# Kernel optimization log

Hardware: AMD Instinct MI355X
Metric: run time of the kernel (lower is better)

## Reference

```python
import jax, jax.numpy as jnp
import numpy as np

D, NH, NKV, HD, DFF, W, PLD = 2048, 8, 2, 256, 8192, 512, 256
EPS = 1e-6

def rmsnorm(x, w):
    # Gemma-style RMSNorm with (1 + weight) scaling
    return x * jax.lax.rsqrt(jnp.mean(x * x, axis=-1, keepdims=True) + EPS) * (1.0 + w)

def rmsnorm_nw(x):
    # v_norm: weightless RMSNorm
    return x * jax.lax.rsqrt(jnp.mean(x * x, axis=-1, keepdims=True) + EPS)

def rotate_half(x):
    x1, x2 = jnp.split(x, 2, axis=-1)
    return jnp.concatenate([-x2, x1], axis=-1)

def setup_inputs() -> dict:
    key = jax.random.key(0)
    ks = jax.random.split(key, 24)
    w = lambda k, shp, s=0.02: (jax.random.normal(k, shp, dtype=jnp.float32) * s)
    inp = {
        "hidden_states": jax.random.normal(ks[0], (1, 1, D), dtype=jnp.float32),
        "cos": jax.random.uniform(ks[1], (1, 1, HD), dtype=jnp.float32),
        "sin": jax.random.uniform(ks[2], (1, 1, HD), dtype=jnp.float32),
        "mask": jnp.zeros((1, 1, 1, W), dtype=jnp.float32),
        "kv_cache": jnp.zeros((2, NKV, W, HD), dtype=jnp.float32),
        "per_layer": jax.random.normal(ks[3], (1, 1, PLD), dtype=jnp.float32),
        "ln_in_w": w(ks[4], (D,)),
        "Wq": w(ks[5], (NH * HD, D)),
        "q_norm_w": w(ks[6], (HD,)),
        "Wk": w(ks[7], (NKV * HD, D)),
        "Wv": w(ks[8], (NKV * HD, D)),
        "k_norm_w": w(ks[9], (HD,)),
        "Wo": w(ks[10], (D, NH * HD)),
        "post_attn_ln_w": w(ks[11], (D,)),
        "pre_ffn_ln_w": w(ks[12], (D,)),
        "Wgate": w(ks[13], (DFF, D)),
        "Wup": w(ks[14], (DFF, D)),
        "Wdown": w(ks[15], (D, DFF)),
        "post_ffn_ln_w": w(ks[16], (D,)),
        "Wpl_gate": w(ks[17], (PLD, D)),
        "Wpl_proj": w(ks[18], (D, PLD)),
        "post_pl_ln_w": w(ks[19], (D,)),
        "layer_scalar": jnp.ones((1,), dtype=jnp.float32),
        "ring_pos": 37,
    }
    return inp

def reference(hidden_states, cos, sin, mask, kv_cache, per_layer,
              ln_in_w, Wq, q_norm_w, Wk, Wv, k_norm_w, Wo,
              post_attn_ln_w, pre_ffn_ln_w, Wgate, Wup, Wdown, post_ffn_ln_w,
              Wpl_gate, Wpl_proj, post_pl_ln_w, layer_scalar, ring_pos):
    n_rep = NH // NKV
    x = hidden_states[0, 0]                      # (D,)
    residual = x
    h = rmsnorm(x, ln_in_w)                      # input_layernorm
    c, s = cos[0, 0], sin[0, 0]                  # (HD,)
    # q/k/v projections (seq=1 decode -> GEMV)
    q = (h @ Wq.T).reshape(NH, HD)
    q = rmsnorm(q, q_norm_w)
    q = q * c + rotate_half(q) * s               # RoPE
    k = (h @ Wk.T).reshape(NKV, HD)
    k = rmsnorm(k, k_norm_w)
    k = k * c + rotate_half(k) * s
    v = rmsnorm_nw((h @ Wv.T).reshape(NKV, HD))
    # slice-write into the ring-buffer KV cache
    kv = kv_cache.at[0, :, ring_pos, :].set(k).at[1, :, ring_pos, :].set(v)
    K, V = kv[0], kv[1]                          # (NKV, W, HD)
    # GQA: repeat kv heads n_rep times
    Kx = jnp.repeat(K, n_rep, axis=0)            # (NH, W, HD)
    Vx = jnp.repeat(V, n_rep, axis=0)
    scores = jnp.einsum('hd,hwd->hw', q, Kx) + mask[0, 0, 0]   # no 1/sqrt(hd), as in source
    attn = jax.nn.softmax(scores, axis=-1)
    o = jnp.einsum('hw,hwd->hd', attn, Vx).reshape(NH * HD)
    attn_out = rmsnorm(o @ Wo.T, post_attn_ln_w)
    x = residual + attn_out
    # gated-GELU MLP
    residual = x
    hn = rmsnorm(x, pre_ffn_ln_w)
    gate = jax.nn.gelu(hn @ Wgate.T, approximate=True)
    mlp = ((gate * (hn @ Wup.T)) @ Wdown.T)
    x = residual + rmsnorm(mlp, post_ffn_ln_w)
    # per-layer input gate/projection
    residual = x
    g = jax.nn.gelu(x @ Wpl_gate.T, approximate=True) * per_layer[0, 0]
    g = rmsnorm(g @ Wpl_proj.T, post_pl_ln_w)
    x = (residual + g) * layer_scalar[0]
    return x.reshape(1, 1, D)

if __name__ == '__main__':
    out = reference(**setup_inputs())
    print(out.shape, out.dtype)
```

## Files before the change

kernel.cpp:

```cpp
#include <hip/hip_runtime.h>
#include <math.h>

#define D 2048
#define NH 8
#define NKV 2
#define HD 256
#define DFF 8192
#define W 512
#define PLD 256
#define EPS 1e-6f

typedef float f32x4 __attribute__((ext_vector_type(4)));

__device__ __forceinline__ f32x4 ntld(const float* p) {
    return __builtin_nontemporal_load(reinterpret_cast<const f32x4*>(p));
}
__device__ __forceinline__ f32x4 ld4(const float* p) {
    return *reinterpret_cast<const f32x4*>(p);
}
__device__ __forceinline__ float dot4(f32x4 a, f32x4 b, float acc) {
    return fmaf(a.x, b.x, fmaf(a.y, b.y, fmaf(a.z, b.z, fmaf(a.w, b.w, acc))));
}

__device__ __forceinline__ float wave_sum(float v) {
    #pragma unroll
    for (int off = 32; off > 0; off >>= 1) v += __shfl_xor(v, off, 64);
    return v;
}
__device__ __forceinline__ float wave_max(float v) {
    #pragma unroll
    for (int off = 32; off > 0; off >>= 1) v = fmaxf(v, __shfl_xor(v, off, 64));
    return v;
}

__device__ __forceinline__ float gelu_tanh(float x) {
    const float c = 0.7978845608028654f;
    float t = tanhf(c * (x + 0.044715f * x * x * x));
    return 0.5f * x * (1.0f + t);
}

__global__ __launch_bounds__(256, 1)
void qkv_fused(const float* __restrict__ Wq, const float* __restrict__ Wk,
               const float* __restrict__ Wv, const float* __restrict__ x,
               const float* __restrict__ lnw, float* __restrict__ qraw,
               float* __restrict__ kraw, float* __restrict__ vraw) {
    int lane = threadIdx.x & 63, wid = threadIdx.x >> 6;
    int row = blockIdx.x * 4 + wid;
    const float* wr;
    float* outp;
    if (row < 2048)      { wr = Wq + (size_t)row * D;          outp = qraw + row; }
    else if (row < 2560) { wr = Wk + (size_t)(row - 2048) * D; outp = kraw + (row - 2048); }
    else                 { wr = Wv + (size_t)(row - 2560) * D; outp = vraw + (row - 2560); }
    f32x4 xv[8], lw[8];
    #pragma unroll
    for (int c = 0; c < 8; c++) xv[c] = ld4(x + c * 256 + lane * 4);
    #pragma unroll
    for (int c = 0; c < 8; c++) lw[c] = ld4(lnw + c * 256 + lane * 4);
    f32x4 wv4[8];
    #pragma unroll
    for (int c = 0; c < 8; c++) wv4[c] = ntld(wr + c * 256 + lane * 4);
    float ss = 0.f;
    #pragma unroll
    for (int c = 0; c < 8; c++) ss = dot4(xv[c], xv[c], ss);
    ss = wave_sum(ss);
    float rs = rsqrtf(ss / (float)D + EPS);
    float acc = 0.f;
    #pragma unroll
    for (int c = 0; c < 8; c++) {
        f32x4 h4 = xv[c] * rs * (1.f + lw[c]);
        acc = dot4(wv4[c], h4, acc);
    }
    acc = wave_sum(acc);
    if (lane == 0) *outp = acc;
}

__global__ __launch_bounds__(1024, 1)
void attn_fused(const float* __restrict__ kvc, const float* __restrict__ qraw,
                const float* __restrict__ kraw, const float* __restrict__ vraw,
                const float* __restrict__ qw, const float* __restrict__ kw,
                const float* __restrict__ cosv, const float* __restrict__ sinv,
                const float* __restrict__ mask, const int* __restrict__ ring_p,
                float* __restrict__ attn_o) {
    __shared__ float qn[HD], kn[HD], vn[HD], p[W], red[16], oacc[4][HD];
    int t = threadIdx.x, wv = t >> 6, lane = t & 63;
    int head = blockIdx.x, kvh = head >> 2;
    int ring = *ring_p;
    if (wv == 0) {
        f32x4 v4 = ld4(qraw + head * HD + lane * 4);
        float ss = wave_sum(dot4(v4, v4, 0.f));
        float rs = rsqrtf(ss / (float)HD + EPS);
        f32x4 w4 = ld4(qw + lane * 4);
        f32x4 nv = v4 * rs * (1.f + w4);
        f32x4 pr;
        pr.x = __shfl_xor(nv.x, 32, 64);
        pr.y = __shfl_xor(nv.y, 32, 64);
        pr.z = __shfl_xor(nv.z, 32, 64);
        pr.w = __shfl_xor(nv.w, 32, 64);
        f32x4 c4 = ld4(cosv + lane * 4), s4 = ld4(sinv + lane * 4);
        float sgn = (lane < 32) ? -1.f : 1.f;
        f32x4 o4 = nv * c4 + pr * s4 * sgn;
        *reinterpret_cast<f32x4*>(qn + lane * 4) = o4;
    } else if (wv == 1) {
        f32x4 v4 = ld4(kraw + kvh * HD + lane * 4);
        float ss = wave_sum(dot4(v4, v4, 0.f));
        float rs = rsqrtf(ss / (float)HD + EPS);
        f32x4 w4 = ld4(kw + lane * 4);
        f32x4 nv = v4 * rs * (1.f + w4);
        f32x4 pr;
        pr.x = __shfl_xor(nv.x, 32, 64);
        pr.y = __shfl_xor(nv.y, 32, 64);
        pr.z = __shfl_xor(nv.z, 32, 64);
        pr.w = __shfl_xor(nv.w, 32, 64);
        f32x4 c4 = ld4(cosv + lane * 4), s4 = ld4(sinv + lane * 4);
        float sgn = (lane < 32) ? -1.f : 1.f;
        f32x4 o4 = nv * c4 + pr * s4 * sgn;
        *reinterpret_cast<f32x4*>(kn + lane * 4) = o4;
    } else if (wv == 2) {
        f32x4 v4 = ld4(vraw + kvh * HD + lane * 4);
        float ss = wave_sum(dot4(v4, v4, 0.f));
        float rs = rsqrtf(ss / (float)HD + EPS);
        *reinterpret_cast<f32x4*>(vn + lane * 4) = v4 * rs;
    }
    __syncthreads();
    {
        f32x4 qq = *reinterpret_cast<f32x4*>(qn + lane * 4);
        f32x4 krg = *reinterpret_cast<f32x4*>(kn + lane * 4);
        const float* Kb = kvc + (size_t)kvh * W * HD;
        #pragma unroll 4
        for (int i = 0; i < 32; i++) {
            int w = wv * 32 + i;
            f32x4 k4 = (w == ring) ? krg : ld4(Kb + (size_t)w * HD + lane * 4);
            float s = wave_sum(dot4(qq, k4, 0.f));
            if (lane == 0) p[w] = s + mask[w];
        }
    }
    __syncthreads();
    float e = 0.f, sv = 0.f;
    if (t < W) {
        sv = p[t];
        float m = wave_max(sv);
        if (lane == 0) red[wv] = m;
    }
    __syncthreads();
    float m = red[0];
    #pragma unroll
    for (int i = 1; i < 8; i++) m = fmaxf(m, red[i]);
    if (t < W) e = expf(sv - m);
    __syncthreads();
    if (t < W) {
        float se = wave_sum(e);
        if (lane == 0) red[wv] = se;
    }
    __syncthreads();
    float tot = 0.f;
    #pragma unroll
    for (int i = 0; i < 8; i++) tot += red[i];
    if (t < W) p[t] = e / tot;
    __syncthreads();
    {
        int d = t & 255, q = t >> 8;
        float vr = vn[d];
        const float* Vb = kvc + (size_t)(NKV + kvh) * W * HD;
        float acc = 0.f;
        #pragma unroll 8
        for (int i = 0; i < 128; i++) {
            int w = q * 128 + i;
            float vv = (w == ring) ? vr : Vb[(size_t)w * HD + d];
            acc = fmaf(p[w], vv, acc);
        }
        oacc[q][d] = acc;
    }
    __syncthreads();
    if (t < HD) attn_o[head * HD + t] = oacc[0][t] + oacc[1][t] + oacc[2][t] + oacc[3][t];
}

__global__ __launch_bounds__(256, 1)
void gemv2048_nt(const float* __restrict__ Wm, const float* __restrict__ x,
                 float* __restrict__ y) {
    int lane = threadIdx.x & 63, wid = threadIdx.x >> 6;
    int row = blockIdx.x * 4 + wid;
    const float* wr = Wm + (size_t)row * D;
    f32x4 xv[8], w[8];
    #pragma unroll
    for (int c = 0; c < 8; c++) xv[c] = ld4(x + c * 256 + lane * 4);
    #pragma unroll
    for (int c = 0; c < 8; c++) w[c] = ntld(wr + c * 256 + lane * 4);
    float acc = 0.f;
    #pragma unroll
    for (int c = 0; c < 8; c++) acc = dot4(w[c], xv[c], acc);
    acc = wave_sum(acc);
    if (lane == 0) y[row] = acc;
}

__global__ __launch_bounds__(256, 1)
void gateup_fused(const float* __restrict__ Wg, const float* __restrict__ Wu,
                  const float* __restrict__ x, const float* __restrict__ ywo,
                  const float* __restrict__ w_pa, const float* __restrict__ w_pf,
                  float* __restrict__ act, float* __restrict__ x1out) {
    int lane = threadIdx.x & 63, wid = threadIdx.x >> 6;
    int row = blockIdx.x * 4 + wid;
    const float* wg = Wg + (size_t)row * D;
    const float* wu = Wu + (size_t)row * D;
    f32x4 y4[8], xr4[8], w1[8], w2[8];
    #pragma unroll
    for (int c = 0; c < 8; c++) y4[c] = ld4(ywo + c * 256 + lane * 4);
    #pragma unroll
    for (int c = 0; c < 8; c++) xr4[c] = ld4(x + c * 256 + lane * 4);
    #pragma unroll
    for (int c = 0; c < 8; c++) w1[c] = ld4(w_pa + c * 256 + lane * 4);
    #pragma unroll
    for (int c = 0; c < 8; c++) w2[c] = ld4(w_pf + c * 256 + lane * 4);
    f32x4 g4[8], u4[8];
    #pragma unroll
    for (int c = 0; c < 8; c++) g4[c] = ntld(wg + c * 256 + lane * 4);
    #pragma unroll
    for (int c = 0; c < 8; c++) u4[c] = ntld(wu + c * 256 + lane * 4);
    float ss = 0.f;
    #pragma unroll
    for (int c = 0; c < 8; c++) ss = dot4(y4[c], y4[c], ss);
    ss = wave_sum(ss);
    float rs1 = rsqrtf(ss / (float)D + EPS);
    f32x4 x1v[8];
    float s2 = 0.f;
    #pragma unroll
    for (int c = 0; c < 8; c++) {
        f32x4 v = xr4[c] + y4[c] * rs1 * (1.f + w1[c]);
        x1v[c] = v;
        s2 = dot4(v, v, s2);
    }
    s2 = wave_sum(s2);
    float rs2 = rsqrtf(s2 / (float)D + EPS);
    if (blockIdx.x == 0 && wid == 0) {
        #pragma unroll
        for (int c = 0; c < 8; c++)
            *reinterpret_cast<f32x4*>(x1out + c * 256 + lane * 4) = x1v[c];
    }
    float ag = 0.f, au = 0.f;
    #pragma unroll
    for (int c = 0; c < 8; c++) {
        f32x4 h4 = x1v[c] * rs2 * (1.f + w2[c]);
        ag = dot4(g4[c], h4, ag);
        au = dot4(u4[c], h4, au);
    }
    ag = wave_sum(ag);
    au = wave_sum(au);
    if (lane == 0) act[row] = gelu_tanh(ag) * au;
}

__global__ __launch_bounds__(256, 1)
void down_nt(const float* __restrict__ Wd, const float* __restrict__ act,
             float* __restrict__ y) {
    int lane = threadIdx.x & 63, wid = threadIdx.x >> 6;
    int row = blockIdx.x * 4 + wid;
    const float* wr = Wd + (size_t)row * DFF;
    f32x4 wA[8], wB[8], a[8];
    float acc = 0.f;
    #pragma unroll
    for (int c = 0; c < 8; c++) a[c] = ld4(act + c * 256 + lane * 4);
    #pragma unroll
    for (int c = 0; c < 8; c++) wA[c] = ntld(wr + c * 256 + lane * 4);
    #pragma unroll
    for (int c = 0; c < 8; c++) wB[c] = ntld(wr + 2048 + c * 256 + lane * 4);
    #pragma unroll
    for (int c = 0; c < 8; c++) acc = dot4(wA[c], a[c], acc);
    #pragma unroll
    for (int c = 0; c < 8; c++) a[c] = ld4(act + 2048 + c * 256 + lane * 4);
    #pragma unroll
    for (int c = 0; c < 8; c++) wA[c] = ntld(wr + 4096 + c * 256 + lane * 4);
    #pragma unroll
    for (int c = 0; c < 8; c++) acc = dot4(wB[c], a[c], acc);
    #pragma unroll
    for (int c = 0; c < 8; c++) a[c] = ld4(act + 4096 + c * 256 + lane * 4);
    #pragma unroll
    for (int c = 0; c < 8; c++) wB[c] = ntld(wr + 6144 + c * 256 + lane * 4);
    #pragma unroll
    for (int c = 0; c < 8; c++) acc = dot4(wA[c], a[c], acc);
    #pragma unroll
    for (int c = 0; c < 8; c++) a[c] = ld4(act + 6144 + c * 256 + lane * 4);
    #pragma unroll
    for (int c = 0; c < 8; c++) acc = dot4(wB[c], a[c], acc);
    acc = wave_sum(acc);
    if (lane == 0) y[row] = acc;
}

__global__ __launch_bounds__(256, 1)
void plgate_fused(const float* __restrict__ Wpl, const float* __restrict__ x1,
                  const float* __restrict__ y2, const float* __restrict__ w_pf,
                  const float* __restrict__ per_layer, float* __restrict__ g,
                  float* __restrict__ x2out) {
    int lane = threadIdx.x & 63, wid = threadIdx.x >> 6;
    int row = blockIdx.x * 4 + wid;
    f32x4 y4[8], x4[8], w4[8];
    #pragma unroll
    for (int c = 0; c < 8; c++) y4[c] = ld4(y2 + c * 256 + lane * 4);
    #pragma unroll
    for (int c = 0; c < 8; c++) x4[c] = ld4(x1 + c * 256 + lane * 4);
    #pragma unroll
    for (int c = 0; c < 8; c++) w4[c] = ld4(w_pf + c * 256 + lane * 4);
    f32x4 wv4[8];
    const float* wr = Wpl + (size_t)row * D;
    #pragma unroll
    for (int c = 0; c < 8; c++) wv4[c] = ntld(wr + c * 256 + lane * 4);
    float ss = 0.f;
    #pragma unroll
    for (int c = 0; c < 8; c++) ss = dot4(y4[c], y4[c], ss);
    ss = wave_sum(ss);
    float rs = rsqrtf(ss / (float)D + EPS);
    f32x4 x2v[8];
    #pragma unroll
    for (int c = 0; c < 8; c++) x2v[c] = x4[c] + y4[c] * rs * (1.f + w4[c]);
    if (blockIdx.x == 0 && wid == 0) {
        #pragma unroll
        for (int c = 0; c < 8; c++)
            *reinterpret_cast<f32x4*>(x2out + c * 256 + lane * 4) = x2v[c];
    }
    float acc = 0.f;
    #pragma unroll
    for (int c = 0; c < 8; c++) acc = dot4(wv4[c], x2v[c], acc);
    acc = wave_sum(acc);
    if (lane == 0) g[row] = gelu_tanh(acc) * per_layer[row];
}

__global__ __launch_bounds__(256, 1)
void gemv256_nt(const float* __restrict__ Wm, const float* __restrict__ x,
                float* __restrict__ y) {
    int lane = threadIdx.x & 63, wid = threadIdx.x >> 6;
    int row = blockIdx.x * 4 + wid;
    f32x4 x0 = ld4(x + lane * 4);
    f32x4 w0 = ntld(Wm + (size_t)row * PLD + lane * 4);
    float acc = dot4(w0, x0, 0.f);
    acc = wave_sum(acc);
    if (lane == 0) y[row] = acc;
}

__global__ __launch_bounds__(256, 1)
void final_fused(const float* __restrict__ x2, const float* __restrict__ g2,
                 const float* __restrict__ w, const float* __restrict__ scal,
                 float* __restrict__ out) {
    int lane = threadIdx.x & 63;
    f32x4 g4[8];
    #pragma unroll
    for (int c = 0; c < 8; c++) g4[c] = ld4(g2 + c * 256 + lane * 4);
    float ss = 0.f;
    #pragma unroll
    for (int c = 0; c < 8; c++) ss = dot4(g4[c], g4[c], ss);
    ss = wave_sum(ss);
    float rs = rsqrtf(ss / (float)D + EPS);
    int idx = blockIdx.x * 256 + threadIdx.x;
    out[idx] = (x2[idx] + g2[idx] * rs * (1.f + w[idx])) * scal[0];
}

extern "C" void kernel_launch(void* const* d_in, const int* in_sizes, int n_in,
                              void* d_out, int out_size, void* d_ws, size_t ws_size,
                              hipStream_t stream) {
    const float* x_in        = (const float*)d_in[0];
    const float* cosv        = (const float*)d_in[1];
    const float* sinv        = (const float*)d_in[2];
    const float* mask        = (const float*)d_in[3];
    const float* kvc         = (const float*)d_in[4];
    const float* per_layer   = (const float*)d_in[5];
    const float* ln_in_w     = (const float*)d_in[6];
    const float* Wq          = (const float*)d_in[7];
    const float* q_norm_w    = (const float*)d_in[8];
    const float* Wk          = (const float*)d_in[9];
    const float* Wv          = (const float*)d_in[10];
    const float* k_norm_w    = (const float*)d_in[11];
    const float* Wo          = (const float*)d_in[12];
    const float* post_attn_w = (const float*)d_in[13];
    const float* pre_ffn_w   = (const float*)d_in[14];
    const float* Wgate       = (const float*)d_in[15];
    const float* Wup         = (const float*)d_in[16];
    const float* Wdown       = (const float*)d_in[17];
    const float* post_ffn_w  = (const float*)d_in[18];
    const float* Wpl_gate    = (const float*)d_in[19];
    const float* Wpl_proj    = (const float*)d_in[20];
    const float* post_pl_w   = (const float*)d_in[21];
    const float* layer_scal  = (const float*)d_in[22];
    const int*   ring_pos    = (const int*)d_in[23];
    float* out = (float*)d_out;
    float* ws  = (float*)d_ws;

    float* qraw   = ws;
    float* kraw   = ws + 2048;
    float* vraw   = ws + 2560;
    float* attn_o = ws + 3072;
    float* y_wo   = ws + 5120;
    float* x1     = ws + 7168;
    float* act    = ws + 9216;
    float* y2     = ws + 17408;
    float* x2     = ws + 19456;
    float* g      = ws + 21504;
    float* g2     = ws + 21760;

    qkv_fused<<<768, 256, 0, stream>>>(Wq, Wk, Wv, x_in, ln_in_w, qraw, kraw, vraw);
    attn_fused<<<8, 1024, 0, stream>>>(kvc, qraw, kraw, vraw, q_norm_w, k_norm_w,
                                       cosv, sinv, mask, ring_pos, attn_o);
    gemv2048_nt<<<512, 256, 0, stream>>>(Wo, attn_o, y_wo);
    gateup_fused<<<2048, 256, 0, stream>>>(Wgate, Wup, x_in, y_wo,
                                           post_attn_w, pre_ffn_w, act, x1);
    down_nt<<<512, 256, 0, stream>>>(Wdown, act, y2);
    plgate_fused<<<64, 256, 0, stream>>>(Wpl_gate, x1, y2, post_ffn_w,
                                         per_layer, g, x2);
    gemv256_nt<<<512, 256, 0, stream>>>(Wpl_proj, g, g2);
    final_fused<<<8, 256, 0, stream>>>(x2, g2, post_pl_w, layer_scal, out);
}
```

Before: 82.17 us.

## Split attention into scores, softmax, and PV kernels across 64 blocks

Replaces the single 8-block attention kernel with three launches: a score kernel spread over 64 blocks (8 window chunks per head), a per-head softmax kernel that also zeroes the output, and a PV kernel over 64 blocks that combines partial sums with atomicAdd. The goal is to use far more compute units to read the KV cache in parallel instead of having only 8 workgroups stream it. In exchange it adds two kernel launches, a global-memory round trip for the scores, and floating-point atomics that make the summation order nondeterministic.

```diff
diff --git a/kernel.cpp b/kernel.cpp
--- a/kernel.cpp
+++ b/kernel.cpp
@@ -74,16 +74,15 @@
     if (lane == 0) *outp = acc;
 }
 
-__global__ __launch_bounds__(1024, 1)
-void attn_fused(const float* __restrict__ kvc, const float* __restrict__ qraw,
-                const float* __restrict__ kraw, const float* __restrict__ vraw,
-                const float* __restrict__ qw, const float* __restrict__ kw,
-                const float* __restrict__ cosv, const float* __restrict__ sinv,
-                const float* __restrict__ mask, const int* __restrict__ ring_p,
-                float* __restrict__ attn_o) {
-    __shared__ float qn[HD], kn[HD], vn[HD], p[W], red[16], oacc[4][HD];
+__global__ __launch_bounds__(256, 1)
+void attn_scores_f(const float* __restrict__ kvc, const float* __restrict__ qraw,
+                   const float* __restrict__ kraw, const float* __restrict__ qw,
+                   const float* __restrict__ kw, const float* __restrict__ cosv,
+                   const float* __restrict__ sinv, const float* __restrict__ mask,
+                   const int* __restrict__ ring_p, float* __restrict__ scores) {
+    __shared__ float qn[HD], kn[HD];
     int t = threadIdx.x, wv = t >> 6, lane = t & 63;
-    int head = blockIdx.x, kvh = head >> 2;
+    int head = blockIdx.x >> 3, wc = blockIdx.x & 7, kvh = head >> 2;
     int ring = *ring_p;
     if (wv == 0) {
         f32x4 v4 = ld4(qraw + head * HD + lane * 4);
@@ -98,8 +97,7 @@
         pr.w = __shfl_xor(nv.w, 32, 64);
         f32x4 c4 = ld4(cosv + lane * 4), s4 = ld4(sinv + lane * 4);
         float sgn = (lane < 32) ? -1.f : 1.f;
-        f32x4 o4 = nv * c4 + pr * s4 * sgn;
-        *reinterpret_cast<f32x4*>(qn + lane * 4) = o4;
+        *reinterpret_cast<f32x4*>(qn + lane * 4) = nv * c4 + pr * s4 * sgn;
     } else if (wv == 1) {
         f32x4 v4 = ld4(kraw + kvh * HD + lane * 4);
         float ss = wave_sum(dot4(v4, v4, 0.f));
@@ -113,65 +111,62 @@
         pr.w = __shfl_xor(nv.w, 32, 64);
         f32x4 c4 = ld4(cosv + lane * 4), s4 = ld4(sinv + lane * 4);
         float sgn = (lane < 32) ? -1.f : 1.f;
-        f32x4 o4 = nv * c4 + pr * s4 * sgn;
-        *reinterpret_cast<f32x4*>(kn + lane * 4) = o4;
-    } else if (wv == 2) {
-        f32x4 v4 = ld4(vraw + kvh * HD + lane * 4);
-        float ss = wave_sum(dot4(v4, v4, 0.f));
-        float rs = rsqrtf(ss / (float)HD + EPS);
-        *reinterpret_cast<f32x4*>(vn + lane * 4) = v4 * rs;
+        *reinterpret_cast<f32x4*>(kn + lane * 4) = nv * c4 + pr * s4 * sgn;
     }
     __syncthreads();
-    {
-        f32x4 qq = *reinterpret_cast<f32x4*>(qn + lane * 4);
-        f32x4 krg = *reinterpret_cast<f32x4*>(kn + lane * 4);
-        const float* Kb = kvc + (size_t)kvh * W * HD;
-        #pragma unroll 4
-        for (int i = 0; i < 32; i++) {
-            int w = wv * 32 + i;
-            f32x4 k4 = (w == ring) ? krg : ld4(Kb + (size_t)w * HD + lane * 4);
-            float s = wave_sum(dot4(qq, k4, 0.f));
-            if (lane == 0) p[w] = s + mask[w];
-        }
-    }
+    f32x4 qq = *reinterpret_cast<f32x4*>(qn + lane * 4);
+    f32x4 krg = *reinterpret_cast<f32x4*>(kn + lane * 4);
+    const float* Kb = kvc + (size_t)kvh * W * HD;
+    #pragma unroll 4
+    for (int i = 0; i < 16; i++) {
+        int w = wc * 64 + wv * 16 + i;
+        f32x4 k4 = (w == ring) ? krg : ld4(Kb + (size_t)w * HD + lane * 4);
+        float s = wave_sum(dot4(qq, k4, 0.f));
+        if (lane == 0) scores[head * W + w] = s + mask[w];
+    }
+}
+
+__global__ __launch_bounds__(256, 1)
+void attn_softmax(float* __restrict__ scores, float* __restrict__ attn_o) {
+    __shared__ float s4[4];
+    int head = blockIdx.x, t = threadIdx.x, lane = t & 63, wv = t >> 6;
+    float s0 = scores[head * W + t], s1 = scores[head * W + 256 + t];
+    float m = wave_max(fmaxf(s0, s1));
+    if (lane == 0) s4[wv] = m;
     __syncthreads();
-    float e = 0.f, sv = 0.f;
-    if (t < W) {
-        sv = p[t];
-        float m = wave_max(sv);
-        if (lane == 0) red[wv] = m;
-    }
+    m = fmaxf(fmaxf(s4[0], s4[1]), fmaxf(s4[2], s4[3]));
     __syncthreads();
-    float m = red[0];
-    #pragma unroll
-    for (int i = 1; i < 8; i++) m = fmaxf(m, red[i]);
-    if (t < W) e = expf(sv - m);
+    float e0 = expf(s0 - m), e1 = expf(s1 - m);
+    float se = wave_sum(e0 + e1);
+    if (lane == 0) s4[wv] = se;
     __syncthreads();
-    if (t < W) {
-        float se = wave_sum(e);
-        if (lane == 0) red[wv] = se;
-    }
-    __syncthreads();
-    float tot = 0.f;
-    #pragma unroll
-    for (int i = 0; i < 8; i++) tot += red[i];
-    if (t < W) p[t] = e / tot;
-    __syncthreads();
-    {
-        int d = t & 255, q = t >> 8;
-        float vr = vn[d];
-        const float* Vb = kvc + (size_t)(NKV + kvh) * W * HD;
-        float acc = 0.f;
-        #pragma unroll 8
-        for (int i = 0; i < 128; i++) {
-            int w = q * 128 + i;
-            float vv = (w == ring) ? vr : Vb[(size_t)w * HD + d];
-            acc = fmaf(p[w], vv, acc);
-        }
-        oacc[q][d] = acc;
-    }
-    __syncthreads();
-    if (t < HD) attn_o[head * HD + t] = oacc[0][t] + oacc[1][t] + oacc[2][t] + oacc[3][t];
+    float tot = s4[0] + s4[1] + s4[2] + s4[3];
+    float inv = 1.f / tot;
+    scores[head * W + t] = e0 * inv;
+    scores[head * W + 256 + t] = e1 * inv;
+    attn_o[head * HD + t] = 0.f;
+}
+
+__global__ __launch_bounds__(256, 1)
+void attn_pv(const float* __restrict__ kvc, const float* __restrict__ vraw,
+             const float* __restrict__ p, const int* __restrict__ ring_p,
+             float* __restrict__ attn_o) {
+    int t = threadIdx.x, lane = t & 63;
+    int head = blockIdx.x >> 3, wc = blockIdx.x & 7, kvh = head >> 2;
+    int ring = *ring_p;
+    f32x4 v4 = ld4(vraw + kvh * HD + lane * 4);
+    float ss = wave_sum(dot4(v4, v4, 0.f));
+    float rs = rsqrtf(ss / (float)HD + EPS);
+    float vr = vraw[kvh * HD + t] * rs;
+    const float* Vb = kvc + (size_t)(NKV + kvh) * W * HD;
+    float acc = 0.f;
+    #pragma unroll 8
+    for (int i = 0; i < 64; i++) {
+        int w = wc * 64 + i;
+        float vv = (w == ring) ? vr : Vb[(size_t)w * HD + t];
+        acc = fmaf(p[head * W + w], vv, acc);
+    }
+    atomicAdd(&attn_o[head * HD + t], acc);
 }
 
 __global__ __launch_bounds__(256, 1)
@@ -383,18 +378,21 @@
     float* qraw   = ws;
     float* kraw   = ws + 2048;
     float* vraw   = ws + 2560;
-    float* attn_o = ws + 3072;
-    float* y_wo   = ws + 5120;
-    float* x1     = ws + 7168;
-    float* act    = ws + 9216;
-    float* y2     = ws + 17408;
-    float* x2     = ws + 19456;
-    float* g      = ws + 21504;
-    float* g2     = ws + 21760;
+    float* scores = ws + 3072;
+    float* attn_o = ws + 7168;
+    float* y_wo   = ws + 9216;
+    float* x1     = ws + 11264;
+    float* act    = ws + 13312;
+    float* y2     = ws + 21504;
+    float* x2     = ws + 23552;
+    float* g      = ws + 25600;
+    float* g2     = ws + 25856;
 
     qkv_fused<<<768, 256, 0, stream>>>(Wq, Wk, Wv, x_in, ln_in_w, qraw, kraw, vraw);
-    attn_fused<<<8, 1024, 0, stream>>>(kvc, qraw, kraw, vraw, q_norm_w, k_norm_w,
-                                       cosv, sinv, mask, ring_pos, attn_o);
+    attn_scores_f<<<64, 256, 0, stream>>>(kvc, qraw, kraw, q_norm_w, k_norm_w,
+                                          cosv, sinv, mask, ring_pos, scores);
+    attn_softmax<<<8, 256, 0, stream>>>(scores, attn_o);
+    attn_pv<<<64, 256, 0, stream>>>(kvc, vraw, scores, ring_pos, attn_o);
     gemv2048_nt<<<512, 256, 0, stream>>>(Wo, attn_o, y_wo);
     gateup_fused<<<2048, 256, 0, stream>>>(Wgate, Wup, x_in, y_wo,
                                            post_attn_w, pre_ffn_w, act, x1);
```

After: 74.71 us. 9.1% less time.
